# Kernel tuning notes

Measured on AMD Instinct MI355X. Metric: run time of the kernel, lower is better.

Reference implementation:

```python
import jax, jax.numpy as jnp
import numpy as np


def setup_inputs() -> dict:
    key = jax.random.key(0)
    k1, k2 = jax.random.split(key)
    B, C, N = 32, 512, 4096
    x = jax.random.normal(k1, (B, C, N), dtype=jnp.float32)
    gamma = jax.random.normal(k2, (1,), dtype=jnp.float32)
    return {"x": x, "gamma": gamma}


def reference(x, gamma):
    # x: [B, C, N]. Channel attention: energy = x @ x^T -> [B, C, C]
    energy = jnp.einsum('bcn,bdn->bcd', x, x)
    # inverted score: rowmax - energy, then softmax over last dim
    energy_new = jnp.max(energy, axis=-1, keepdims=True) - energy
    attention = jax.nn.softmax(energy_new, axis=-1)  # [B, C, C]
    out = jnp.einsum('bcd,bdn->bcn', attention, x)
    return gamma * out + x
```

## Files before the change

### kernel.cpp

```cpp
#include <hip/hip_runtime.h>
#include <stdint.h>
#include <stddef.h>

#define NB 32
#define NC 512
#define NN 4096
#define NSPLIT 4
#define KCH (NN / NSPLIT)

typedef _Float16 h4_t __attribute__((ext_vector_type(4)));
typedef _Float16 h8_t __attribute__((ext_vector_type(8)));
typedef float    f4_t __attribute__((ext_vector_type(4)));

__device__ __forceinline__ void gload16(const _Float16* g, _Float16* l) {
    __builtin_amdgcn_global_load_lds(
        (const __attribute__((address_space(1))) void*)g,
        (__attribute__((address_space(3))) void*)l, 16, 0, 0);
}


__global__ __launch_bounds__(256) void cast_transpose(
    const float* __restrict__ x, _Float16* __restrict__ Xh,
    _Float16* __restrict__ Xl, _Float16* __restrict__ Xt)
{
    __shared__ __attribute__((aligned(16))) _Float16 tile[64 * 66];
    const int b = blockIdx.z, c0 = blockIdx.y * 64, n0 = blockIdx.x * 64;
    const int t = threadIdx.x;
    const int lr = t >> 4;
    const int lc = (t & 15) * 4;
    const size_t xbase = (size_t)b * NC * NN;

#pragma unroll
    for (int p = 0; p < 4; ++p) {
        const int r = p * 16 + lr;
        const size_t off = xbase + (size_t)(c0 + r) * NN + (n0 + lc);
        const float4 v = *(const float4*)(x + off);
        const _Float16 h0 = (_Float16)v.x, h1 = (_Float16)v.y;
        const _Float16 h2 = (_Float16)v.z, h3 = (_Float16)v.w;
        h4_t hv = {h0, h1, h2, h3};
        *(h4_t*)(Xh + off) = hv;
        h4_t lv = {(_Float16)(v.x - (float)h0), (_Float16)(v.y - (float)h1),
                   (_Float16)(v.z - (float)h2), (_Float16)(v.w - (float)h3)};
        *(h4_t*)(Xl + off) = lv;
        tile[r * 66 + lc + 0] = h0;
        tile[r * 66 + lc + 1] = h1;
        tile[r * 66 + lc + 2] = h2;
        tile[r * 66 + lc + 3] = h3;
    }
    __syncthreads();
    const size_t tbase = (size_t)b * NN * NC;
#pragma unroll
    for (int p = 0; p < 4; ++p) {
        const int rn = p * 16 + lr;
        h4_t w;
        w[0] = tile[(lc + 0) * 66 + rn];
        w[1] = tile[(lc + 1) * 66 + rn];
        w[2] = tile[(lc + 2) * 66 + rn];
        w[3] = tile[(lc + 3) * 66 + rn];
        *(h4_t*)(Xt + tbase + (size_t)(n0 + rn) * NC + (c0 + lc)) = w;
    }
}

__global__ __launch_bounds__(256) void cast_hl(
    const float* __restrict__ x, _Float16* __restrict__ Xh,
    _Float16* __restrict__ Xl)
{
    const size_t total = (size_t)NB * NC * NN / 4;
    for (size_t i = (size_t)blockIdx.x * 256 + threadIdx.x; i < total;
         i += (size_t)gridDim.x * 256) {
        const float4 v = ((const float4*)x)[i];
        const _Float16 h0 = (_Float16)v.x, h1 = (_Float16)v.y;
        const _Float16 h2 = (_Float16)v.z, h3 = (_Float16)v.w;
        h4_t hv = {h0, h1, h2, h3};
        h4_t lv = {(_Float16)(v.x - (float)h0), (_Float16)(v.y - (float)h1),
                   (_Float16)(v.z - (float)h2), (_Float16)(v.w - (float)h3)};
        ((h4_t*)Xh)[i] = hv;
        ((h4_t*)Xl)[i] = lv;
    }
}

__global__ __launch_bounds__(256, 4) void gemm1_energy(
    const _Float16* __restrict__ Xh, const _Float16* __restrict__ Xl,
    float* __restrict__ part)
{
    __shared__ __attribute__((aligned(16))) _Float16 sAh[128 * 32];
    __shared__ __attribute__((aligned(16))) _Float16 sBh[128 * 32];
    __shared__ __attribute__((aligned(16))) _Float16 sAl[128 * 32];
    __shared__ __attribute__((aligned(16))) _Float16 sBl[128 * 32];

    const int flat = blockIdx.x;
    const int xcd  = flat & 7;
    const int slot = flat >> 3;
    const int grp  = xcd + 8 * (slot / 10);
    const int mem  = slot % 10;
    const int b    = grp >> 2;
    const int s    = grp & (NSPLIT - 1);

    const int ti = (int)((sqrtf(8.0f * (float)mem + 1.0f) - 1.0f) * 0.5f);
    const int tj = mem - ((ti * (ti + 1)) >> 1);
    const bool diag = (ti == tj);

    const int t = threadIdx.x;
    const int wave = t >> 6, lane = t & 63;
    const int srow = t >> 2;
    const int scol = (((t & 3) ^ ((t >> 3) & 3)) * 8);

    const size_t xb = (size_t)b * NC * NN + (size_t)s * KCH;
    const _Float16* gAh = Xh + xb + (size_t)(ti * 128 + srow) * NN + scol;
    const _Float16* gBh = Xh + xb + (size_t)(tj * 128 + srow) * NN + scol;
    const _Float16* gAl = Xl + xb + (size_t)(ti * 128 + srow) * NN + scol;
    const _Float16* gBl = Xl + xb + (size_t)(tj * 128 + srow) * NN + scol;

    const int wr = wave >> 1, wc = wave & 1;
    const int fr = lane & 15, fko = (lane >> 4) * 8;
    const int hi4 = (lane >> 4) * 4;
    const int fsw = fko ^ (((fr >> 1) & 3) << 3);

    const _Float16* rBh = diag ? sAh : sBh;
    const _Float16* rBl = diag ? sAl : sBl;

    f4_t acc[4][4];
#pragma unroll
    for (int m = 0; m < 4; ++m)
#pragma unroll
        for (int n = 0; n < 4; ++n) acc[m][n] = (f4_t){0.f, 0.f, 0.f, 0.f};

    for (int k0 = 0; k0 < KCH; k0 += 32) {
        gload16(gAh + k0,                   sAh + wave * 512);
        gload16(gAh + k0 + 64 * (size_t)NN, sAh + 2048 + wave * 512);
        gload16(gAl + k0,                   sAl + wave * 512);
        gload16(gAl + k0 + 64 * (size_t)NN, sAl + 2048 + wave * 512);
        if (!diag) {
            gload16(gBh + k0,                   sBh + wave * 512);
            gload16(gBh + k0 + 64 * (size_t)NN, sBh + 2048 + wave * 512);
            gload16(gBl + k0,                   sBl + wave * 512);
            gload16(gBl + k0 + 64 * (size_t)NN, sBl + 2048 + wave * 512);
        }
        __syncthreads();

        h8_t ah[4], bh[4], al[4], bl[4];
#pragma unroll
        for (int m = 0; m < 4; ++m) {
            ah[m] = *(const h8_t*)(sAh + (wr * 64 + m * 16 + fr) * 32 + fsw);
            bh[m] = *(const h8_t*)(rBh + (wc * 64 + m * 16 + fr) * 32 + fsw);
            al[m] = *(const h8_t*)(sAl + (wr * 64 + m * 16 + fr) * 32 + fsw);
            bl[m] = *(const h8_t*)(rBl + (wc * 64 + m * 16 + fr) * 32 + fsw);
        }
#pragma unroll
        for (int m = 0; m < 4; ++m)
#pragma unroll
            for (int nf = 0; nf < 4; ++nf) {
                acc[nf][m] = __builtin_amdgcn_mfma_f32_16x16x32_f16(bh[nf], ah[m], acc[nf][m], 0, 0, 0);
                acc[nf][m] = __builtin_amdgcn_mfma_f32_16x16x32_f16(bl[nf], ah[m], acc[nf][m], 0, 0, 0);
                acc[nf][m] = __builtin_amdgcn_mfma_f32_16x16x32_f16(bh[nf], al[m], acc[nf][m], 0, 0, 0);
            }
        __syncthreads();
    }

    float* pb = part + ((size_t)s * NB + b) * (NC * NC);
#pragma unroll
    for (int m = 0; m < 4; ++m) {
        const int i = ti * 128 + wr * 64 + m * 16 + fr;
#pragma unroll
        for (int nf = 0; nf < 4; ++nf) {
            const int jjb = tj * 128 + wc * 64 + nf * 16 + hi4;
            *(f4_t*)(pb + (size_t)i * NC + jjb) = acc[nf][m];
            if (!diag) {
#pragma unroll
                for (int j = 0; j < 4; ++j)
                    pb[(size_t)(jjb + j) * NC + i] = acc[nf][m][j];
            }
        }
    }
}

__global__ __launch_bounds__(256) void softmax_inv(
    const float* __restrict__ part, _Float16* __restrict__ attn)
{
    const int row = blockIdx.x * 4 + (threadIdx.x >> 6);
    const int lane = threadIdx.x & 63;
    const size_t roff = (size_t)row * NC;

    float4 a0 = {0.f, 0.f, 0.f, 0.f}, a1 = {0.f, 0.f, 0.f, 0.f};
#pragma unroll
    for (int s = 0; s < NSPLIT; ++s) {
        const float4* p = (const float4*)(part + (size_t)s * NB * NC * NC + roff);
        const float4 v0 = p[lane], v1 = p[64 + lane];
        a0.x += v0.x; a0.y += v0.y; a0.z += v0.z; a0.w += v0.w;
        a1.x += v1.x; a1.y += v1.y; a1.z += v1.z; a1.w += v1.w;
    }

    float mn = fminf(fminf(fminf(a0.x, a0.y), fminf(a0.z, a0.w)),
                     fminf(fminf(a1.x, a1.y), fminf(a1.z, a1.w)));
#pragma unroll
    for (int off = 32; off; off >>= 1) mn = fminf(mn, __shfl_xor(mn, off));

    const float w0 = __expf(mn - a0.x), w1 = __expf(mn - a0.y);
    const float w2 = __expf(mn - a0.z), w3 = __expf(mn - a0.w);
    const float w4 = __expf(mn - a1.x), w5 = __expf(mn - a1.y);
    const float w6 = __expf(mn - a1.z), w7 = __expf(mn - a1.w);
    float sum = ((w0 + w1) + (w2 + w3)) + ((w4 + w5) + (w6 + w7));
#pragma unroll
    for (int off = 32; off; off >>= 1) sum += __shfl_xor(sum, off);
    const float inv = 1.0f / sum;

    h4_t o0 = {(_Float16)(w0 * inv), (_Float16)(w1 * inv),
               (_Float16)(w2 * inv), (_Float16)(w3 * inv)};
    h4_t o1 = {(_Float16)(w4 * inv), (_Float16)(w5 * inv),
               (_Float16)(w6 * inv), (_Float16)(w7 * inv)};
    ((h4_t*)(attn + roff))[lane] = o0;
    ((h4_t*)(attn + roff))[64 + lane] = o1;
}

__global__ __launch_bounds__(256) void transpose_h(
    const _Float16* __restrict__ Xh, _Float16* __restrict__ Xt)
{
    __shared__ __attribute__((aligned(16))) _Float16 tile[64 * 66];
    const int b = blockIdx.z, c0 = blockIdx.y * 64, n0 = blockIdx.x * 64;
    const int t = threadIdx.x;
    const int lr = t >> 4;
    const int lc = (t & 15) * 4;
    const size_t hbase = (size_t)b * NC * NN;

#pragma unroll
    for (int p = 0; p < 4; ++p) {
        const int r = p * 16 + lr;
        const h4_t v = *(const h4_t*)(Xh + hbase + (size_t)(c0 + r) * NN + (n0 + lc));
        tile[r * 66 + lc + 0] = v[0];
        tile[r * 66 + lc + 1] = v[1];
        tile[r * 66 + lc + 2] = v[2];
        tile[r * 66 + lc + 3] = v[3];
    }
    __syncthreads();
    const size_t tbase = (size_t)b * NN * NC;
#pragma unroll
    for (int p = 0; p < 4; ++p) {
        const int rn = p * 16 + lr;
        h4_t w;
        w[0] = tile[(lc + 0) * 66 + rn];
        w[1] = tile[(lc + 1) * 66 + rn];
        w[2] = tile[(lc + 2) * 66 + rn];
        w[3] = tile[(lc + 3) * 66 + rn];
        *(h4_t*)(Xt + tbase + (size_t)(n0 + rn) * NC + (c0 + lc)) = w;
    }
}

__global__ __launch_bounds__(256) void gemm2_out(
    const _Float16* __restrict__ attn, const _Float16* __restrict__ Xt,
    const _Float16* __restrict__ Xh, const float* __restrict__ gammap,
    float* __restrict__ out)
{
    __shared__ __attribute__((aligned(16))) _Float16 sA[128 * 32];
    __shared__ __attribute__((aligned(16))) _Float16 sB[128 * 32];

    const int flat = blockIdx.x;
    const int xcd  = flat & 7;
    const int slot = flat >> 3;
    const int b    = xcd + 8 * (slot >> 7);
    const int memb = slot & 127;
    const int brow = (memb & 3) * 128;
    const int bcol = (memb >> 2) * 128;

    const int t = threadIdx.x;
    const int wave = t >> 6, lane = t & 63;
    const int srow = t >> 2;
    const int scol = (((t & 3) ^ ((t >> 3) & 3)) * 8);

    const _Float16* gA = attn + (size_t)b * NC * NC + (size_t)(brow + srow) * NC + scol;
    const _Float16* gB = Xt   + (size_t)b * NN * NC + (size_t)(bcol + srow) * NC + scol;

    const int wr = wave >> 1, wc = wave & 1;
    const int fr = lane & 15, fko = (lane >> 4) * 8;
    const int hi4 = (lane >> 4) * 4;
    const int fsw = fko ^ (((fr >> 1) & 3) << 3);

    f4_t acc[4][4];
#pragma unroll
    for (int m = 0; m < 4; ++m)
#pragma unroll
        for (int n = 0; n < 4; ++n) acc[m][n] = (f4_t){0.f, 0.f, 0.f, 0.f};

    for (int k0 = 0; k0 < NC; k0 += 32) {
        gload16(gA + k0,           sA + wave * 512);
        gload16(gA + k0 + 64 * NC, sA + 2048 + wave * 512);
        gload16(gB + k0,           sB + wave * 512);
        gload16(gB + k0 + 64 * NC, sB + 2048 + wave * 512);
        __syncthreads();

        h8_t a[4], bb[4];
#pragma unroll
        for (int m = 0; m < 4; ++m) {
            a[m]  = *(const h8_t*)(sA + (wr * 64 + m * 16 + fr) * 32 + fsw);
            bb[m] = *(const h8_t*)(sB + (wc * 64 + m * 16 + fr) * 32 + fsw);
        }
#pragma unroll
        for (int m = 0; m < 4; ++m)
#pragma unroll
            for (int nf = 0; nf < 4; ++nf)
                acc[nf][m] = __builtin_amdgcn_mfma_f32_16x16x32_f16(bb[nf], a[m], acc[nf][m], 0, 0, 0);
        __syncthreads();
    }

    const float g = gammap[0];
    const _Float16* xb = Xh + (size_t)b * NC * NN;
    float* ob = out + (size_t)b * NC * NN;
#pragma unroll
    for (int m = 0; m < 4; ++m) {
        const int c_ = brow + wr * 64 + m * 16 + fr;
#pragma unroll
        for (int nf = 0; nf < 4; ++nf) {
            const int n_ = bcol + wc * 64 + nf * 16 + hi4;
            const size_t off = (size_t)c_ * NN + n_;
            const h4_t xv = *(const h4_t*)(xb + off);
            f4_t o;
#pragma unroll
            for (int j = 0; j < 4; ++j)
                o[j] = g * acc[nf][m][j] + (float)xv[j];
            *(f4_t*)(ob + off) = o;
        }
    }
}

extern "C" void kernel_launch(void* const* d_in, const int* in_sizes, int n_in,
                              void* d_out, int out_size, void* d_ws, size_t ws_size,
                              hipStream_t stream)
{
    const float* x     = (const float*)d_in[0];
    const float* gamma = (const float*)d_in[1];
    float* out = (float*)d_out;
    char* ws = (char*)d_ws;

    if (ws_size >= 553648128ull) {
        _Float16* Xh   = (_Float16*)(ws);
        _Float16* Xl   = (_Float16*)(ws + 134217728ull);
        _Float16* Xt   = (_Float16*)(ws + 268435456ull);
        _Float16* attn = (_Float16*)(ws + 402653184ull);
        float*    part = (float*)   (ws + 419430400ull);

        cast_transpose<<<dim3(NN / 64, NC / 64, NB), 256, 0, stream>>>(x, Xh, Xl, Xt);
        gemm1_energy<<<dim3(10 * NSPLIT * NB), 256, 0, stream>>>(Xh, Xl, part);
        softmax_inv<<<dim3(NB * NC / 4), 256, 0, stream>>>(part, attn);
        gemm2_out<<<dim3(4096), 256, 0, stream>>>(attn, Xt, Xh, gamma, out);
    } else {
        _Float16* Xh   = (_Float16*)(ws);
        _Float16* XlXt = (_Float16*)(ws + 134217728ull);
        _Float16* attn = (_Float16*)(ws + 268435456ull);
        float*    part = (float*)   (ws + 285212672ull);

        cast_hl<<<dim3(2048), 256, 0, stream>>>(x, Xh, XlXt);
        gemm1_energy<<<dim3(10 * NSPLIT * NB), 256, 0, stream>>>(Xh, XlXt, part);
        softmax_inv<<<dim3(NB * NC / 4), 256, 0, stream>>>(part, attn);
        transpose_h<<<dim3(NN / 64, NC / 64, NB), 256, 0, stream>>>(Xh, XlXt);
        gemm2_out<<<dim3(4096), 256, 0, stream>>>(attn, XlXt, Xh, gamma, out);
    }
}
```

Baseline: 476.6 us.

## Triple-buffer LDS in gemm2_out with async prefetch two stages ahead

Replaces the single-buffered load-sync-compute loop in the second GEMM with a 3-stage LDS ring. Global-to-LDS loads for stage k+2 are issued while stage k is computed, gated by vmcnt waits and a single barrier per iteration. The goal is to hide global memory latency behind MFMA work and drop one barrier per K step. The cost is three times the LDS footprint (48KB), which may reduce occupancy.

```diff
diff --git a/kernel.cpp b/kernel.cpp
--- a/kernel.cpp
+++ b/kernel.cpp
@@ -250,8 +250,8 @@
     const _Float16* __restrict__ Xh, const float* __restrict__ gammap,
     float* __restrict__ out)
 {
-    __shared__ __attribute__((aligned(16))) _Float16 sA[128 * 32];
-    __shared__ __attribute__((aligned(16))) _Float16 sB[128 * 32];
+    __shared__ __attribute__((aligned(16))) _Float16 sA[3][128 * 32];
+    __shared__ __attribute__((aligned(16))) _Float16 sB[3][128 * 32];
 
     const int flat = blockIdx.x;
     const int xcd  = flat & 7;
@@ -263,16 +263,14 @@
 
     const int t = threadIdx.x;
     const int wave = t >> 6, lane = t & 63;
-    const int srow = t >> 2;
-    const int scol = (((t & 3) ^ ((t >> 3) & 3)) * 8);
-
-    const _Float16* gA = attn + (size_t)b * NC * NC + (size_t)(brow + srow) * NC + scol;
-    const _Float16* gB = Xt   + (size_t)b * NN * NC + (size_t)(bcol + srow) * NC + scol;
-
     const int wr = wave >> 1, wc = wave & 1;
-    const int fr = lane & 15, fko = (lane >> 4) * 8;
-    const int hi4 = (lane >> 4) * 4;
-    const int fsw = fko ^ (((fr >> 1) & 3) << 3);
+    const int fr = lane & 15, fq = lane >> 4;
+    const int hi4 = fq * 4;
+
+    const int rr = t >> 2;
+    const int sck = (((t & 3) ^ ((rr >> 1) & 3)) * 8);
+    const _Float16* gA = attn + (size_t)b * NC * NC + (size_t)brow * NC;
+    const _Float16* gB = Xt   + (size_t)b * NN * NC + (size_t)bcol * NC;
 
     f4_t acc[4][4];
 #pragma unroll
@@ -280,26 +278,45 @@
 #pragma unroll
         for (int n = 0; n < 4; ++n) acc[m][n] = (f4_t){0.f, 0.f, 0.f, 0.f};
 
-    for (int k0 = 0; k0 < NC; k0 += 32) {
-        gload16(gA + k0,           sA + wave * 512);
-        gload16(gA + k0 + 64 * NC, sA + 2048 + wave * 512);
-        gload16(gB + k0,           sB + wave * 512);
-        gload16(gB + k0 + 64 * NC, sB + 2048 + wave * 512);
-        __syncthreads();
-
-        h8_t a[4], bb[4];
+#define STG2(buf, k0)                                                         \
+    {                                                                         \
+        gload16(gA + (size_t)rr * NC + (k0) + sck,        &sA[buf][0] + t * 8); \
+        gload16(gA + (size_t)(64 + rr) * NC + (k0) + sck, &sA[buf][0] + 2048 + t * 8); \
+        gload16(gB + (size_t)rr * NC + (k0) + sck,        &sB[buf][0] + t * 8); \
+        gload16(gB + (size_t)(64 + rr) * NC + (k0) + sck, &sB[buf][0] + 2048 + t * 8); \
+    }
+
+    STG2(0, 0);
+    STG2(1, 32);
+
+#pragma unroll
+    for (int it = 0; it < 16; ++it) {
+        if (it < 15) {
+            asm volatile("s_waitcnt vmcnt(4)" ::: "memory");
+        } else {
+            asm volatile("s_waitcnt vmcnt(0)" ::: "memory");
+        }
+        __builtin_amdgcn_s_barrier();
+        if (it + 2 < 16) STG2((it + 2) % 3, (it + 2) * 32);
+
+        const _Float16* cA = &sA[it % 3][0];
+        const _Float16* cB = &sB[it % 3][0];
+        h8_t a_[4], b_[4];
 #pragma unroll
         for (int m = 0; m < 4; ++m) {
-            a[m]  = *(const h8_t*)(sA + (wr * 64 + m * 16 + fr) * 32 + fsw);
-            bb[m] = *(const h8_t*)(sB + (wc * 64 + m * 16 + fr) * 32 + fsw);
+            const int ar = wr * 64 + m * 16 + fr;
+            const int br = wc * 64 + m * 16 + fr;
+            a_[m] = *(const h8_t*)(cA + ar * 32 + ((fq ^ ((ar >> 1) & 3)) * 8));
+            b_[m] = *(const h8_t*)(cB + br * 32 + ((fq ^ ((br >> 1) & 3)) * 8));
         }
 #pragma unroll
         for (int m = 0; m < 4; ++m)
 #pragma unroll
             for (int nf = 0; nf < 4; ++nf)
-                acc[nf][m] = __builtin_amdgcn_mfma_f32_16x16x32_f16(bb[nf], a[m], acc[nf][m], 0, 0, 0);
-        __syncthreads();
-    }
+                acc[nf][m] = __builtin_amdgcn_mfma_f32_16x16x32_f16(
+                    b_[nf], a_[m], acc[nf][m], 0, 0, 0);
+    }
+#undef STG2
 
     const float g = gammap[0];
     const _Float16* xb = Xh + (size_t)b * NC * NN;
```

Result: faster. 465.3 us (-2.4%).
